# Kernel optimization log

Measured on AMD Instinct MI355X. Metric: run time of the kernel, lower is better.

The kernel has to match this reference:

```python
import jax, jax.numpy as jnp
import numpy as np

N, P, D, C = 2048, 64, 512, 32   # bs*n_vars, patch_num, hidden_dim, cluster_num
H, DFF, L = 8, 2048, 3           # heads, ffn dim, encoder layers
TEMP = 10.0
EPS = 1e-10
LN_EPS = 1e-5


def setup_inputs() -> dict:
    key = jax.random.key(0)
    ks = jax.random.split(key, 18)
    s = 0.02  # small init to keep activations sane
    inp = {}
    inp["input_series"] = jax.random.normal(ks[0], (N, P, D), jnp.float32)
    pi = jax.random.uniform(ks[1], (C,), jnp.float32) + 0.1
    inp["text_pi"] = pi / pi.sum()
    A = jax.random.uniform(ks[2], (C, C), jnp.float32) + 0.1
    inp["text_A"] = A / A.sum(axis=1, keepdims=True)
    # stacked per-layer TransformerEncoderLayer params (torch post-norm, relu)
    inp["qkv_w"] = jax.random.normal(ks[3], (L, 3 * D, D), jnp.float32) * s
    inp["qkv_b"] = jnp.zeros((L, 3 * D), jnp.float32)
    inp["out_w"] = jax.random.normal(ks[4], (L, D, D), jnp.float32) * s
    inp["out_b"] = jnp.zeros((L, D), jnp.float32)
    inp["ln1_w"] = jnp.ones((L, D), jnp.float32)
    inp["ln1_b"] = jnp.zeros((L, D), jnp.float32)
    inp["ff1_w"] = jax.random.normal(ks[5], (L, DFF, D), jnp.float32) * s
    inp["ff1_b"] = jnp.zeros((L, DFF), jnp.float32)
    inp["ff2_w"] = jax.random.normal(ks[6], (L, D, DFF), jnp.float32) * s
    inp["ff2_b"] = jnp.zeros((L, D), jnp.float32)
    inp["ln2_w"] = jnp.ones((L, D), jnp.float32)
    inp["ln2_b"] = jnp.zeros((L, D), jnp.float32)
    inp["mus"] = jax.random.normal(ks[7], (C, D), jnp.float32)
    return inp


def _layer_norm(x, w, b):
    m = x.mean(axis=-1, keepdims=True)
    v = ((x - m) ** 2).mean(axis=-1, keepdims=True)
    return (x - m) * jax.lax.rsqrt(v + LN_EPS) * w + b


def _encoder_layer(x, qkv_w, qkv_b, out_w, out_b, ln1_w, ln1_b,
                   ff1_w, ff1_b, ff2_w, ff2_b, ln2_w, ln2_b):
    n, p, d = x.shape
    dh = d // H
    qkv = x @ qkv_w.T + qkv_b                       # [n,p,3d]
    q, k, v = jnp.split(qkv, 3, axis=-1)
    def split_heads(t):
        return t.reshape(n, p, H, dh).transpose(0, 2, 1, 3)  # [n,h,p,dh]
    q, k, v = split_heads(q), split_heads(k), split_heads(v)
    scores = jnp.einsum('nhqd,nhkd->nhqk', q, k) / (dh ** 0.5)
    attn = jax.nn.softmax(scores, axis=-1)
    o = jnp.einsum('nhqk,nhkd->nhqd', attn, v)
    o = o.transpose(0, 2, 1, 3).reshape(n, p, d)
    o = o @ out_w.T + out_b
    x = _layer_norm(x + o, ln1_w, ln1_b)            # post-norm
    f = jax.nn.relu(x @ ff1_w.T + ff1_b) @ ff2_w.T + ff2_b
    return _layer_norm(x + f, ln2_w, ln2_b)


def reference(input_series, text_pi, text_A, qkv_w, qkv_b, out_w, out_b,
              ln1_w, ln1_b, ff1_w, ff1_b, ff2_w, ff2_b, ln2_w, ln2_b, mus):
    x = input_series
    for l in range(L):
        x = _encoder_layer(x, qkv_w[l], qkv_b[l], out_w[l], out_b[l],
                           ln1_w[l], ln1_b[l], ff1_w[l], ff1_b[l],
                           ff2_w[l], ff2_b[l], ln2_w[l], ln2_b[l])
    emb_ts = x                                       # [N,P,D]
    # ClusterCenters: softmax of exp(-||x - tanh(mu)||^2 / T)
    mu = jnp.tanh(mus)                               # [C,D]
    dist = ((emb_ts ** 2).sum(-1)[..., None]
            + (mu ** 2).sum(-1)[None, None, :]
            - 2.0 * jnp.einsum('npd,cd->npc', emb_ts, mu))  # [N,P,C]
    z = jnp.exp(-dist / TEMP)
    logits_all = z / z.sum(axis=-1, keepdims=True)
    log_za = jnp.log(logits_all + EPS)               # [N,P,C]
    # sequential HMM-style recursion over patches
    l0 = jax.nn.softmax(jnp.log(text_pi + EPS)[None, :] + log_za[:, 0], axis=-1)
    def step(c, lz):
        c2 = jax.nn.softmax(jnp.log(c @ text_A + EPS) + lz, axis=-1)
        return c2, c2
    _, ys = jax.lax.scan(step, l0, jnp.swapaxes(log_za[:, 1:], 0, 1))  # [P-1,N,C]
    cluster_probs = jnp.concatenate([l0[:, None], jnp.swapaxes(ys, 0, 1)], axis=1)
    entropy_loss = -jnp.sum(cluster_probs * jnp.log(cluster_probs + EPS), axis=-1).mean()
    return (cluster_probs, emb_ts, text_pi, text_A, entropy_loss)
```

## Files before the change

kernel.cpp:

```cpp
#include <hip/hip_runtime.h>
#include <stdint.h>


typedef __bf16 bf16;
typedef __bf16 bf16x2 __attribute__((ext_vector_type(2)));
typedef __bf16 bf16x4 __attribute__((ext_vector_type(4)));
typedef __bf16 bf16x8 __attribute__((ext_vector_type(8)));
typedef float  f32x4  __attribute__((ext_vector_type(4)));
typedef float  f32x2  __attribute__((ext_vector_type(2)));

#define EPSF 1e-10f
#define NROWS 131072L

__device__ __forceinline__ float bflo(uint32_t u){ return __uint_as_float(u << 16); }
__device__ __forceinline__ float bfhi(uint32_t u){ return __uint_as_float(u & 0xffff0000u); }

__device__ __forceinline__ void gload_lds16(const bf16* g, bf16* l){
  __builtin_amdgcn_global_load_lds((const __attribute__((address_space(1))) uint32_t*)g,
                                   (__attribute__((address_space(3))) uint32_t*)l,
                                   16, 0, 0);
}

__global__ void k_f2bf(const float* __restrict__ in, bf16* __restrict__ out, long n){
  const long stride = (long)gridDim.x * blockDim.x * 4;
  for (long i = ((long)blockIdx.x * blockDim.x + threadIdx.x) * 4; i < n; i += stride){
    f32x4 v = *(const f32x4*)(in + i);
    bf16x4 o = { (bf16)v[0], (bf16)v[1], (bf16)v[2], (bf16)v[3] };
    *(bf16x4*)(out + i) = o;
  }
}


#define MFMA_HALF(RH)                                                         \
  {                                                                           \
    __builtin_amdgcn_s_setprio(1);                                            \
    _Pragma("unroll")                                                         \
    for (int kk = 0; kk < 2; kk++) {                                          \
      _Pragma("unroll")                                                       \
      for (int i2 = 0; i2 < 4; i2++) {                                        \
        _Pragma("unroll")                                                     \
        for (int jj = 0; jj < 4; jj++) {                                      \
          acc[(RH)*4+i2][jj] = __builtin_amdgcn_mfma_f32_16x16x32_bf16(       \
              a[i2][kk], b[jj][kk], acc[(RH)*4+i2][jj], 0, 0, 0);             \
        }                                                                     \
      }                                                                       \
    }                                                                         \
    __builtin_amdgcn_s_setprio(0);                                            \
  }

#define RD_A(RH)                                                              \
  _Pragma("unroll")                                                           \
  for (int i2 = 0; i2 < 4; i2++) {                                            \
    a[i2][0] = *(const bf16x8*)&Ac[(aRow + (RH)*64 + i2*16) * 64 + sl0];      \
    a[i2][1] = *(const bf16x8*)&Ac[(aRow + (RH)*64 + i2*16) * 64 + sl1];      \
  }

#define RD_B_ALL                                                              \
  _Pragma("unroll")                                                           \
  for (int jj = 0; jj < 4; jj++) {                                            \
    b[jj][0] = *(const bf16x8*)&Bc[(bRow + jj*16) * 64 + sl0];                \
    b[jj][1] = *(const bf16x8*)&Bc[(bRow + jj*16) * 64 + sl1];                \
  }

#define ISSUE_A(dst, BI, KK) \
  gload_lds16(gA + (long)(BI)*64*lda + (KK), (dst) + (BI)*4096 + wslice)
#define ISSUE_B(dst, BI, KK) \
  gload_lds16(gB + (long)(BI)*64*K   + (KK), (dst) + (BI)*4096 + wslice)

#define WAITV(N)  asm volatile("s_waitcnt vmcnt(" #N ")" ::: "memory")
#define WAITL0    asm volatile("s_waitcnt lgkmcnt(0)" ::: "memory")
#define BARRIER   { __builtin_amdgcn_s_barrier(); asm volatile("" ::: "memory"); }

template<int RELU>
__global__ __launch_bounds__(512, 2)
void gemm256(const bf16* __restrict__ A, long lda,
             const bf16* __restrict__ W,
             const float* __restrict__ bias,
             bf16* __restrict__ Cb, long K, int nbx)
{
  const int tid  = threadIdx.x;
  const int wid  = tid >> 6;
  const int lane = tid & 63;
  const int wr = wid >> 2, wc = wid & 3;
  const long ldc = (long)nbx * 256;

  const unsigned nwg = gridDim.x;
  const unsigned q   = nwg >> 3;
  const unsigned swz = (blockIdx.x & 7) * q + (blockIdx.x >> 3);
  const unsigned bx  = swz % (unsigned)nbx;
  const unsigned by  = swz / (unsigned)nbx;
  const long bm = (long)by * 256;
  const long bn = (long)bx * 256;

  __shared__ __align__(16) bf16 smem[65536];
  bf16* const As0 = smem;
  bf16* const Bs0 = smem + 16384;
  bf16* const As1 = smem + 32768;
  bf16* const Bs1 = smem + 49152;

  const int srow   = wid * 8 + (lane >> 3);
  const int scol   = ((lane & 7) ^ ((lane >> 3) & 7)) * 8;
  const int wslice = wid * 512;
  const bf16* gA = A + (bm + srow) * lda + scol;
  const bf16* gB = W + (bn + srow) * K   + scol;

  const int fr = lane & 15, fg = lane >> 4;
  const int aRow = wr * 128 + fr;
  const int bRow = wc * 64  + fr;
  const int sl0 = ((0 + fg) ^ (fr & 7)) * 8;
  const int sl1 = ((4 + fg) ^ (fr & 7)) * 8;

  f32x4 acc[8][4];
#pragma unroll
  for (int i = 0; i < 8; i++)
#pragma unroll
    for (int j = 0; j < 4; j++) acc[i][j] = (f32x4){0.f, 0.f, 0.f, 0.f};

  bf16x8 a[4][2];
  bf16x8 b[4][2];

  const int nt = (int)(K >> 6);

  ISSUE_B(Bs0, 0, 0); ISSUE_B(Bs0, 1, 0); ISSUE_B(Bs0, 2, 0); ISSUE_B(Bs0, 3, 0);
  ISSUE_A(As0, 0, 0); ISSUE_A(As0, 2, 0);
  ISSUE_A(As0, 1, 0); ISSUE_A(As0, 3, 0);
  WAITV(2);
  BARRIER;

  for (int t = 0; t < nt; t++){
    bf16* const Ac = (t & 1) ? As1 : As0;
    bf16* const Bc = (t & 1) ? Bs1 : Bs0;
    bf16* const An = (t & 1) ? As0 : As1;
    bf16* const Bn = (t & 1) ? Bs0 : Bs1;
    const bool stage = (t + 1 < nt);
    const long kn = (long)(t + 1) << 6;

    RD_A(0); RD_B_ALL;
    if (stage){ ISSUE_B(Bn, 0, kn); ISSUE_B(Bn, 1, kn);
                ISSUE_B(Bn, 2, kn); ISSUE_B(Bn, 3, kn);
                ISSUE_A(An, 0, kn); ISSUE_A(An, 2, kn); }
    WAITL0;
    MFMA_HALF(0);
    if (stage){ WAITV(6); } else { WAITV(0); }
    BARRIER;

    RD_A(1);
    if (stage){ ISSUE_A(An, 1, kn); ISSUE_A(An, 3, kn); }
    WAITL0;
    MFMA_HALF(1);
    if (stage){ WAITV(2); }
    BARRIER;
  }

  bf16* const cw = smem + wid * 2304;
  const long strip_row0 = bm + wr * 128;
  const long strip_col0 = bn + wc * 64;
  float bv[4];
#pragma unroll
  for (int j = 0; j < 4; j++) bv[j] = bias[strip_col0 + j * 16 + fr];
  const int rrow = lane >> 3;
  const int rcol = (lane & 7) * 8;

#pragma unroll
  for (int ch = 0; ch < 4; ch++){
#pragma unroll
    for (int i2 = 0; i2 < 2; i2++){
      const int i = ch * 2 + i2;
#pragma unroll
      for (int j = 0; j < 4; j++){
#pragma unroll
        for (int r = 0; r < 4; r++){
          float v = acc[i][j][r] + bv[j];
          if (RELU) v = fmaxf(v, 0.f);
          cw[(i2 * 16 + fg * 4 + r) * 72 + j * 16 + fr] = (bf16)v;
        }
      }
    }
    WAITL0;
#pragma unroll
    for (int p = 0; p < 4; p++){
      const int row = p * 8 + rrow;
      bf16x8 o = *(const bf16x8*)&cw[row * 72 + rcol];
      *(bf16x8*)&Cb[(strip_row0 + ch * 32 + row) * ldc + strip_col0 + rcol] = o;
    }
    WAITL0;
  }
}

__global__ __launch_bounds__(256)
void attention(bf16* __restrict__ qkv)
{
  const int blk = blockIdx.x;
  const long n = blk >> 3;
  const int h  = blk & 7;
  const int tid = threadIdx.x;
  const int wid = tid >> 6, lane = tid & 63;

  __shared__ __align__(16) bf16 Qs[64][72];
  __shared__ __align__(16) bf16 Ks[64][72];
  __shared__ __align__(16) bf16 Vt[64][72];

  bf16* base = qkv + n * 64 * 1536 + h * 64;

  for (int c = tid; c < 512; c += 256){
    const int row = c >> 3, col = (c & 7) * 8;
    const long go = (long)row * 1536 + col;
    *(bf16x8*)&Qs[row][col] = *(const bf16x8*)(base + go);
    *(bf16x8*)&Ks[row][col] = *(const bf16x8*)(base + 512 + go);
    bf16x8 v = *(const bf16x8*)(base + 1024 + go);
#pragma unroll
    for (int e = 0; e < 8; e++) Vt[col + e][row] = v[e];
  }
  __syncthreads();

  const int fr = lane & 15, fg = lane >> 4;
  f32x4 sacc[4];
#pragma unroll
  for (int j = 0; j < 4; j++) sacc[j] = (f32x4){0.f, 0.f, 0.f, 0.f};
#pragma unroll
  for (int ks = 0; ks < 2; ks++){
    bf16x8 aa = *(const bf16x8*)&Qs[wid * 16 + fr][ks * 32 + fg * 8];
#pragma unroll
    for (int j = 0; j < 4; j++){
      bf16x8 bb = *(const bf16x8*)&Ks[j * 16 + fr][ks * 32 + fg * 8];
      sacc[j] = __builtin_amdgcn_mfma_f32_16x16x32_bf16(aa, bb, sacc[j], 0, 0, 0);
    }
  }

  float pv[4][4];
#pragma unroll
  for (int r = 0; r < 4; r++){
    float m = -1e30f;
#pragma unroll
    for (int j = 0; j < 4; j++) m = fmaxf(m, sacc[j][r]);
#pragma unroll
    for (int msk = 1; msk < 16; msk <<= 1) m = fmaxf(m, __shfl_xor(m, msk));
    float s = 0.f;
#pragma unroll
    for (int j = 0; j < 4; j++){
      float p = __expf((sacc[j][r] - m) * 0.125f);
      pv[j][r] = p; s += p;
    }
#pragma unroll
    for (int msk = 1; msk < 16; msk <<= 1) s += __shfl_xor(s, msk);
    const float inv = 1.f / s;
#pragma unroll
    for (int j = 0; j < 4; j++) pv[j][r] *= inv;
  }

#pragma unroll
  for (int j = 0; j < 4; j++)
#pragma unroll
    for (int r = 0; r < 4; r++)
      Qs[wid * 16 + fg * 4 + r][j * 16 + fr] = (bf16)pv[j][r];
  __syncthreads();

  f32x4 oacc[4];
#pragma unroll
  for (int j = 0; j < 4; j++) oacc[j] = (f32x4){0.f, 0.f, 0.f, 0.f};
#pragma unroll
  for (int ks = 0; ks < 2; ks++){
    bf16x8 aa = *(const bf16x8*)&Qs[wid * 16 + fr][ks * 32 + fg * 8];
#pragma unroll
    for (int j = 0; j < 4; j++){
      bf16x8 bb = *(const bf16x8*)&Vt[j * 16 + fr][ks * 32 + fg * 8];
      oacc[j] = __builtin_amdgcn_mfma_f32_16x16x32_bf16(aa, bb, oacc[j], 0, 0, 0);
    }
  }
#pragma unroll
  for (int j = 0; j < 4; j++)
#pragma unroll
    for (int r = 0; r < 4; r++)
      base[(long)(wid * 16 + fg * 4 + r) * 1536 + j * 16 + fr] = (bf16)oacc[j][r];
}

__global__ __launch_bounds__(256)
void resid_ln(const bf16* __restrict__ X, const bf16* __restrict__ O,
              const float* __restrict__ w, const float* __restrict__ b,
              bf16* __restrict__ Y, float* __restrict__ EF)
{
  const int wid = threadIdx.x >> 6, lane = threadIdx.x & 63;
  const long row = (long)blockIdx.x * 4 + wid;
  const uint4 xu = ((const uint4*)(X + row * 512))[lane];
  const uint4 ou = ((const uint4*)(O + row * 512))[lane];
  float s[8];
  s[0] = bflo(xu.x) + bflo(ou.x);  s[1] = bfhi(xu.x) + bfhi(ou.x);
  s[2] = bflo(xu.y) + bflo(ou.y);  s[3] = bfhi(xu.y) + bfhi(ou.y);
  s[4] = bflo(xu.z) + bflo(ou.z);  s[5] = bfhi(xu.z) + bfhi(ou.z);
  s[6] = bflo(xu.w) + bflo(ou.w);  s[7] = bfhi(xu.w) + bfhi(ou.w);
  float sum = 0.f, sq = 0.f;
#pragma unroll
  for (int e = 0; e < 8; e++){ sum += s[e]; sq += s[e] * s[e]; }
#pragma unroll
  for (int m = 1; m < 64; m <<= 1){ sum += __shfl_xor(sum, m); sq += __shfl_xor(sq, m); }
  const float mean = sum * (1.f / 512.f);
  const float var  = sq * (1.f / 512.f) - mean * mean;
  const float rs   = rsqrtf(var + 1e-5f);
  const f32x4 w0 = *(const f32x4*)(w + 8 * lane);
  const f32x4 w1 = *(const f32x4*)(w + 8 * lane + 4);
  const f32x4 b0 = *(const f32x4*)(b + 8 * lane);
  const f32x4 b1 = *(const f32x4*)(b + 8 * lane + 4);
  float o[8];
#pragma unroll
  for (int e = 0; e < 4; e++) o[e]     = (s[e]     - mean) * rs * w0[e] + b0[e];
#pragma unroll
  for (int e = 0; e < 4; e++) o[e + 4] = (s[e + 4] - mean) * rs * w1[e] + b1[e];
  bf16x8 ov = { (bf16)o[0], (bf16)o[1], (bf16)o[2], (bf16)o[3],
                (bf16)o[4], (bf16)o[5], (bf16)o[6], (bf16)o[7] };
  *(bf16x8*)(Y + row * 512 + 8 * lane) = ov;
  if (EF){
    f32x4 e0 = { o[0], o[1], o[2], o[3] };
    f32x4 e1 = { o[4], o[5], o[6], o[7] };
    *(f32x4*)(EF + row * 512 + 8 * lane) = e0;
    *(f32x4*)(EF + row * 512 + 8 * lane + 4) = e1;
  }
}

__global__ __launch_bounds__(256)
void k_mu(const float* __restrict__ mus, bf16* __restrict__ mubf, float* __restrict__ munorm)
{
  const int c = blockIdx.x, tid = threadIdx.x, lane = tid & 63, wid = tid >> 6;
  const f32x2 v = *(const f32x2*)(mus + c * 512 + 2 * tid);
  const float t0 = tanhf(v[0]), t1 = tanhf(v[1]);
  bf16x2 o2 = { (bf16)t0, (bf16)t1 };
  *(bf16x2*)(mubf + c * 512 + 2 * tid) = o2;
  float sq = t0 * t0 + t1 * t1;
#pragma unroll
  for (int m = 1; m < 64; m <<= 1) sq += __shfl_xor(sq, m);
  __shared__ float red[4];
  if (lane == 0) red[wid] = sq;
  __syncthreads();
  if (tid == 0) munorm[c] = red[0] + red[1] + red[2] + red[3];
}

__global__ __launch_bounds__(256)
void cluster_logza(const bf16* __restrict__ X, const bf16* __restrict__ MU,
                   const float* __restrict__ munorm, float* __restrict__ out)
{
  const int tid = threadIdx.x, lane = tid & 63, wid = tid >> 6;
  __shared__ __align__(16) bf16 mus[32][512];
  __shared__ float xs[512];
  __shared__ float red[4];
  __shared__ float dots[32];
  for (int c = tid; c < 2048; c += 256){
    const int r = c >> 6, col = (c & 63) * 8;
    *(bf16x8*)&mus[r][col] = *(const bf16x8*)(MU + r * 512 + col);
  }
  const int cc = tid >> 3, seg = tid & 7;
  const long row0 = (long)blockIdx.x * 16;
  __syncthreads();
  for (int rr = 0; rr < 16; rr++){
    const long row = row0 + rr;
    const uint32_t u = ((const uint32_t*)(X + row * 512))[tid];
    const float aa = bflo(u), bb = bfhi(u);
    xs[2 * tid] = aa; xs[2 * tid + 1] = bb;
    float sq = aa * aa + bb * bb;
#pragma unroll
    for (int m = 1; m < 64; m <<= 1) sq += __shfl_xor(sq, m);
    if (lane == 0) red[wid] = sq;
    __syncthreads();
    const float xn = red[0] + red[1] + red[2] + red[3];
    float p = 0.f;
#pragma unroll
    for (int jj = 0; jj < 8; jj++){
      const int col = jj * 64 + seg * 8;
      bf16x8 m8 = *(const bf16x8*)&mus[cc][col];
      const float* xv = &xs[col];
#pragma unroll
      for (int e = 0; e < 8; e++) p += xv[e] * (float)m8[e];
    }
#pragma unroll
    for (int m = 1; m < 8; m <<= 1) p += __shfl_xor(p, m);
    if (seg == 0) dots[cc] = p;
    __syncthreads();
    if (tid < 32){
      const float dist = xn + munorm[tid] - 2.f * dots[tid];
      const float lg = -dist * 0.1f;
      float mx = lg;
#pragma unroll
      for (int m = 1; m < 32; m <<= 1) mx = fmaxf(mx, __shfl_xor(mx, m, 32));
      const float z = __expf(lg - mx);
      float s = z;
#pragma unroll
      for (int m = 1; m < 32; m <<= 1) s += __shfl_xor(s, m, 32);
      out[row * 32 + tid] = logf(z / s + EPSF);
    }
    __syncthreads();
  }
}

__global__ __launch_bounds__(256)
void k_hmm(const float* __restrict__ lza, const float* __restrict__ pi,
           const float* __restrict__ A, float* __restrict__ cp, float* __restrict__ ent)
{
  __shared__ float As[32][33];
  const int tid = threadIdx.x;
  for (int i = tid; i < 1024; i += 256) As[i >> 5][i & 31] = A[i];
  __syncthreads();
  const int j = tid & 31;
  const long n = (long)blockIdx.x * 8 + (tid >> 5);
  const float* lz = lza + n * 2048;

  float c = logf(pi[j] + EPSF) + lz[j];
  {
    float mx = c;
#pragma unroll
    for (int m = 1; m < 32; m <<= 1) mx = fmaxf(mx, __shfl_xor(mx, m, 32));
    float z = __expf(c - mx), s = z;
#pragma unroll
    for (int m = 1; m < 32; m <<= 1) s += __shfl_xor(s, m, 32);
    c = z / s;
  }
  cp[n * 2048 + j] = c;
  float ea = -c * logf(c + EPSF);

  for (int p = 1; p < 64; p++){
    float y = 0.f;
#pragma unroll
    for (int i = 0; i < 32; i++) y += __shfl(c, i, 32) * As[i][j];
    float t = logf(y + EPSF) + lz[p * 32 + j];
    float mx = t;
#pragma unroll
    for (int m = 1; m < 32; m <<= 1) mx = fmaxf(mx, __shfl_xor(mx, m, 32));
    float z = __expf(t - mx), s = z;
#pragma unroll
    for (int m = 1; m < 32; m <<= 1) s += __shfl_xor(s, m, 32);
    c = z / s;
    cp[n * 2048 + p * 32 + j] = c;
    ea += -c * logf(c + EPSF);
  }
#pragma unroll
  for (int m = 1; m < 32; m <<= 1) ea += __shfl_xor(ea, m, 32);
  if (j == 0) atomicAdd(ent, ea * (1.f / 131072.f));
}

extern "C" void kernel_launch(void* const* d_in, const int* in_sizes, int n_in,
                              void* d_out, int out_size, void* d_ws, size_t ws_size,
                              hipStream_t stream)
{
  (void)in_sizes; (void)n_in; (void)out_size; (void)ws_size;
  const float* in_series = (const float*)d_in[0];
  const float* pi    = (const float*)d_in[1];
  const float* Amat  = (const float*)d_in[2];
  const float* qkv_w = (const float*)d_in[3];
  const float* qkv_b = (const float*)d_in[4];
  const float* out_w = (const float*)d_in[5];
  const float* out_b = (const float*)d_in[6];
  const float* ln1_w = (const float*)d_in[7];
  const float* ln1_b = (const float*)d_in[8];
  const float* ff1_w = (const float*)d_in[9];
  const float* ff1_b = (const float*)d_in[10];
  const float* ff2_w = (const float*)d_in[11];
  const float* ff2_b = (const float*)d_in[12];
  const float* ln2_w = (const float*)d_in[13];
  const float* ln2_b = (const float*)d_in[14];
  const float* mus   = (const float*)d_in[15];

  char* ws = (char*)d_ws;
  bf16* region0 = (bf16*)(ws);
  bf16* xb      = (bf16*)(ws + 536870912L);
  bf16* oproj   = (bf16*)(ws + 671088640L);
  bf16* w_qkv   = (bf16*)(ws + 805306368L);
  bf16* w_out   = (bf16*)(ws + 810024960L);
  bf16* w_ff1   = (bf16*)(ws + 811597824L);
  bf16* w_ff2   = (bf16*)(ws + 817889280L);
  bf16* mubf    = (bf16*)(ws + 824180736L);
  float* munorm = (float*)(ws + 824213504L);
  float* logza  = (float*)(ws);

  float* out_f = (float*)d_out;
  float* cp    = out_f;
  float* emb   = out_f + 4194304L;
  float* o_pi  = out_f + 71303168L;
  float* o_A   = out_f + 71303200L;
  float* o_ent = out_f + 71304224L;

  k_f2bf<<<8192, 256, 0, stream>>>(in_series, xb, 67108864L);
  k_f2bf<<<1024, 256, 0, stream>>>(qkv_w, w_qkv, 2359296L);
  k_f2bf<<<1024, 256, 0, stream>>>(out_w, w_out, 786432L);
  k_f2bf<<<1024, 256, 0, stream>>>(ff1_w, w_ff1, 3145728L);
  k_f2bf<<<1024, 256, 0, stream>>>(ff2_w, w_ff2, 3145728L);
  k_mu<<<32, 256, 0, stream>>>(mus, mubf, munorm);

  for (int l = 0; l < 3; l++){
    gemm256<0><<<3072, 512, 0, stream>>>(xb, 512, w_qkv + (long)l * 786432L,
                                         qkv_b + (long)l * 1536, region0, 512, 6);
    attention<<<16384, 256, 0, stream>>>(region0);
    gemm256<0><<<1024, 512, 0, stream>>>(region0, 1536, w_out + (long)l * 262144L,
                                         out_b + (long)l * 512, oproj, 512, 2);
    resid_ln<<<32768, 256, 0, stream>>>(xb, oproj, ln1_w + (long)l * 512,
                                        ln1_b + (long)l * 512, xb, nullptr);
    gemm256<1><<<4096, 512, 0, stream>>>(xb, 512, w_ff1 + (long)l * 1048576L,
                                         ff1_b + (long)l * 2048, region0, 512, 8);
    gemm256<0><<<1024, 512, 0, stream>>>(region0, 2048, w_ff2 + (long)l * 1048576L,
                                         ff2_b + (long)l * 512, oproj, 2048, 2);
    resid_ln<<<32768, 256, 0, stream>>>(xb, oproj, ln2_w + (long)l * 512,
                                        ln2_b + (long)l * 512, xb,
                                        (l == 2) ? emb : nullptr);
  }

  cluster_logza<<<8192, 256, 0, stream>>>(xb, mubf, munorm, logza);
  hipMemsetAsync(o_ent, 0, 4, stream);
  k_hmm<<<256, 256, 0, stream>>>(logza, pi, Amat, cp, o_ent);
  hipMemcpyAsync(o_pi, pi, 32 * sizeof(float), hipMemcpyDeviceToDevice, stream);
  hipMemcpyAsync(o_A, Amat, 1024 * sizeof(float), hipMemcpyDeviceToDevice, stream);
}
```

Measured before the change: 3.963 ms.

## Use 4 waves with 128x128 warp tiles in the 256x256 GEMM

The 256x256 GEMM block goes from 8 waves (each 128x64) to 4 waves (each 128x128), so each wave holds a 8x8 grid of MFMA accumulators and reuses every A fragment across twice as many B fragments. The global-to-LDS staging is reorganised so each wave issues its own set of row chunks, with new vmcnt wait counts, and the epilogue staging buffer is widened. The aim is fewer LDS reads per MFMA. In exchange it raises register pressure (256 accumulator floats per lane) and drops occupancy to one 256-thread block per CU, which risks less latency hiding.

```diff
diff --git a/kernel.cpp b/kernel.cpp
--- a/kernel.cpp
+++ b/kernel.cpp
@@ -31,7 +31,7 @@
 }
 
 
-#define MFMA_HALF(RH)                                                         \
+#define MFMA_BLK(IB)                                                          \
   {                                                                           \
     __builtin_amdgcn_s_setprio(1);                                            \
     _Pragma("unroll")                                                         \
@@ -39,9 +39,9 @@
       _Pragma("unroll")                                                       \
       for (int i2 = 0; i2 < 4; i2++) {                                        \
         _Pragma("unroll")                                                     \
-        for (int jj = 0; jj < 4; jj++) {                                      \
-          acc[(RH)*4+i2][jj] = __builtin_amdgcn_mfma_f32_16x16x32_bf16(       \
-              a[i2][kk], b[jj][kk], acc[(RH)*4+i2][jj], 0, 0, 0);             \
+        for (int j2 = 0; j2 < 8; j2++) {                                      \
+          acc[(IB)*4+i2][j2] = __builtin_amdgcn_mfma_f32_16x16x32_bf16(       \
+              a[i2][kk], b[j2][kk], acc[(IB)*4+i2][j2], 0, 0, 0);             \
         }                                                                     \
       }                                                                       \
     }                                                                         \
@@ -51,28 +51,28 @@
 #define RD_A(RH)                                                              \
   _Pragma("unroll")                                                           \
   for (int i2 = 0; i2 < 4; i2++) {                                            \
-    a[i2][0] = *(const bf16x8*)&Ac[(aRow + (RH)*64 + i2*16) * 64 + sl0];      \
-    a[i2][1] = *(const bf16x8*)&Ac[(aRow + (RH)*64 + i2*16) * 64 + sl1];      \
+    a[i2][0] = *(const bf16x8*)&Ac[aOff + ((RH)*4 + i2)*1024 + sl0];          \
+    a[i2][1] = *(const bf16x8*)&Ac[aOff + ((RH)*4 + i2)*1024 + sl1];          \
   }
 
 #define RD_B_ALL                                                              \
   _Pragma("unroll")                                                           \
-  for (int jj = 0; jj < 4; jj++) {                                            \
-    b[jj][0] = *(const bf16x8*)&Bc[(bRow + jj*16) * 64 + sl0];                \
-    b[jj][1] = *(const bf16x8*)&Bc[(bRow + jj*16) * 64 + sl1];                \
-  }
-
-#define ISSUE_A(dst, BI, KK) \
-  gload_lds16(gA + (long)(BI)*64*lda + (KK), (dst) + (BI)*4096 + wslice)
-#define ISSUE_B(dst, BI, KK) \
-  gload_lds16(gB + (long)(BI)*64*K   + (KK), (dst) + (BI)*4096 + wslice)
+  for (int j2 = 0; j2 < 8; j2++) {                                            \
+    b[j2][0] = *(const bf16x8*)&Bc[bOff + j2*1024 + sl0];                     \
+    b[j2][1] = *(const bf16x8*)&Bc[bOff + j2*1024 + sl1];                     \
+  }
+
+#define ISSUE_A(dst, C, KK) \
+  gload_lds16(gA + (long)(C)*8*lda + (KK), (dst) + (C)*512)
+#define ISSUE_B(dst, C, KK) \
+  gload_lds16(gB + (long)(C)*8*K   + (KK), (dst) + (C)*512)
 
 #define WAITV(N)  asm volatile("s_waitcnt vmcnt(" #N ")" ::: "memory")
 #define WAITL0    asm volatile("s_waitcnt lgkmcnt(0)" ::: "memory")
 #define BARRIER   { __builtin_amdgcn_s_barrier(); asm volatile("" ::: "memory"); }
 
 template<int RELU>
-__global__ __launch_bounds__(512, 2)
+__global__ __launch_bounds__(256, 1)
 void gemm256(const bf16* __restrict__ A, long lda,
              const bf16* __restrict__ W,
              const float* __restrict__ bias,
@@ -81,7 +81,7 @@
   const int tid  = threadIdx.x;
   const int wid  = tid >> 6;
   const int lane = tid & 63;
-  const int wr = wid >> 2, wc = wid & 3;
+  const int wr = wid >> 1, wc = wid & 1;
   const long ldc = (long)nbx * 256;
 
   const unsigned nwg = gridDim.x;
@@ -98,33 +98,37 @@
   bf16* const As1 = smem + 32768;
   bf16* const Bs1 = smem + 49152;
 
-  const int srow   = wid * 8 + (lane >> 3);
-  const int scol   = ((lane & 7) ^ ((lane >> 3) & 7)) * 8;
-  const int wslice = wid * 512;
-  const bf16* gA = A + (bm + srow) * lda + scol;
-  const bf16* gB = W + (bn + srow) * K   + scol;
+  const int gsrc = ((lane & 7) ^ ((lane >> 3) & 7)) * 8;
+  const bf16* gA = A + (bm + (lane >> 3)) * lda + gsrc;
+  const bf16* gB = W + (bn + (lane >> 3)) * K   + gsrc;
+
+  const int cA0[4] = { 2*wid, 2*wid + 1, 16 + 2*wid, 17 + 2*wid };
+  const int cA1[4] = { 8 + 2*wid, 9 + 2*wid, 24 + 2*wid, 25 + 2*wid };
 
   const int fr = lane & 15, fg = lane >> 4;
-  const int aRow = wr * 128 + fr;
-  const int bRow = wc * 64  + fr;
+  const int aOff = (wr * 128 + fr) * 64;
+  const int bOff = (wc * 128 + fr) * 64;
   const int sl0 = ((0 + fg) ^ (fr & 7)) * 8;
   const int sl1 = ((4 + fg) ^ (fr & 7)) * 8;
 
-  f32x4 acc[8][4];
+  f32x4 acc[8][8];
 #pragma unroll
   for (int i = 0; i < 8; i++)
 #pragma unroll
-    for (int j = 0; j < 4; j++) acc[i][j] = (f32x4){0.f, 0.f, 0.f, 0.f};
+    for (int j = 0; j < 8; j++) acc[i][j] = (f32x4){0.f, 0.f, 0.f, 0.f};
 
   bf16x8 a[4][2];
-  bf16x8 b[4][2];
+  bf16x8 b[8][2];
 
   const int nt = (int)(K >> 6);
 
-  ISSUE_B(Bs0, 0, 0); ISSUE_B(Bs0, 1, 0); ISSUE_B(Bs0, 2, 0); ISSUE_B(Bs0, 3, 0);
-  ISSUE_A(As0, 0, 0); ISSUE_A(As0, 2, 0);
-  ISSUE_A(As0, 1, 0); ISSUE_A(As0, 3, 0);
-  WAITV(2);
+#pragma unroll
+  for (int u = 0; u < 4; u++) ISSUE_A(As0, cA0[u], 0);
+#pragma unroll
+  for (int u = 0; u < 8; u++) ISSUE_B(Bs0, 8*wid + u, 0);
+#pragma unroll
+  for (int u = 0; u < 4; u++) ISSUE_A(As0, cA1[u], 0);
+  WAITV(4);
   BARRIER;
 
   for (int t = 0; t < nt; t++){
@@ -136,30 +140,32 @@
     const long kn = (long)(t + 1) << 6;
 
     RD_A(0); RD_B_ALL;
-    if (stage){ ISSUE_B(Bn, 0, kn); ISSUE_B(Bn, 1, kn);
-                ISSUE_B(Bn, 2, kn); ISSUE_B(Bn, 3, kn);
-                ISSUE_A(An, 0, kn); ISSUE_A(An, 2, kn); }
-    WAITL0;
-    MFMA_HALF(0);
-    if (stage){ WAITV(6); } else { WAITV(0); }
+    if (stage){
+#pragma unroll
+      for (int u = 0; u < 4; u++) ISSUE_A(An, cA0[u], kn);
+#pragma unroll
+      for (int u = 0; u < 8; u++) ISSUE_B(Bn, 8*wid + u, kn);
+    }
+    MFMA_BLK(0);
+    if (stage){ WAITV(12); } else { WAITV(0); }
     BARRIER;
 
     RD_A(1);
-    if (stage){ ISSUE_A(An, 1, kn); ISSUE_A(An, 3, kn); }
-    WAITL0;
-    MFMA_HALF(1);
-    if (stage){ WAITV(2); }
+    if (stage){
+#pragma unroll
+      for (int u = 0; u < 4; u++) ISSUE_A(An, cA1[u], kn);
+    }
+    MFMA_BLK(1);
+    if (stage){ WAITV(4); } else { WAITV(0); }
     BARRIER;
   }
 
-  bf16* const cw = smem + wid * 2304;
-  const long strip_row0 = bm + wr * 128;
-  const long strip_col0 = bn + wc * 64;
-  float bv[4];
-#pragma unroll
-  for (int j = 0; j < 4; j++) bv[j] = bias[strip_col0 + j * 16 + fr];
-  const int rrow = lane >> 3;
-  const int rcol = (lane & 7) * 8;
+  bf16* const cw = smem + wid * 4352;
+  const long r0 = bm + wr * 128;
+  const long c0 = bn + wc * 128;
+  float bv[8];
+#pragma unroll
+  for (int j = 0; j < 8; j++) bv[j] = bias[c0 + j * 16 + fr];
 
 #pragma unroll
   for (int ch = 0; ch < 4; ch++){
@@ -167,21 +173,21 @@
     for (int i2 = 0; i2 < 2; i2++){
       const int i = ch * 2 + i2;
 #pragma unroll
-      for (int j = 0; j < 4; j++){
+      for (int j = 0; j < 8; j++){
 #pragma unroll
         for (int r = 0; r < 4; r++){
           float v = acc[i][j][r] + bv[j];
           if (RELU) v = fmaxf(v, 0.f);
-          cw[(i2 * 16 + fg * 4 + r) * 72 + j * 16 + fr] = (bf16)v;
+          cw[(i2 * 16 + fg * 4 + r) * 136 + j * 16 + fr] = (bf16)v;
         }
       }
     }
     WAITL0;
 #pragma unroll
-    for (int p = 0; p < 4; p++){
-      const int row = p * 8 + rrow;
-      bf16x8 o = *(const bf16x8*)&cw[row * 72 + rcol];
-      *(bf16x8*)&Cb[(strip_row0 + ch * 32 + row) * ldc + strip_col0 + rcol] = o;
+    for (int p = 0; p < 8; p++){
+      const int row = p * 4 + fg;
+      bf16x8 o = *(const bf16x8*)&cw[row * 136 + fr * 8];
+      *(bf16x8*)&Cb[(r0 + ch * 32 + row) * ldc + c0 + fr * 8] = o;
     }
     WAITL0;
   }
@@ -483,16 +489,16 @@
   k_mu<<<32, 256, 0, stream>>>(mus, mubf, munorm);
 
   for (int l = 0; l < 3; l++){
-    gemm256<0><<<3072, 512, 0, stream>>>(xb, 512, w_qkv + (long)l * 786432L,
+    gemm256<0><<<3072, 256, 0, stream>>>(xb, 512, w_qkv + (long)l * 786432L,
                                          qkv_b + (long)l * 1536, region0, 512, 6);
     attention<<<16384, 256, 0, stream>>>(region0);
-    gemm256<0><<<1024, 512, 0, stream>>>(region0, 1536, w_out + (long)l * 262144L,
+    gemm256<0><<<1024, 256, 0, stream>>>(region0, 1536, w_out + (long)l * 262144L,
                                          out_b + (long)l * 512, oproj, 512, 2);
     resid_ln<<<32768, 256, 0, stream>>>(xb, oproj, ln1_w + (long)l * 512,
                                         ln1_b + (long)l * 512, xb, nullptr);
-    gemm256<1><<<4096, 512, 0, stream>>>(xb, 512, w_ff1 + (long)l * 1048576L,
+    gemm256<1><<<4096, 256, 0, stream>>>(xb, 512, w_ff1 + (long)l * 1048576L,
                                          ff1_b + (long)l * 2048, region0, 512, 8);
-    gemm256<0><<<1024, 512, 0, stream>>>(region0, 2048, w_ff2 + (long)l * 1048576L,
+    gemm256<0><<<1024, 256, 0, stream>>>(region0, 2048, w_ff2 + (long)l * 1048576L,
                                          ff2_b + (long)l * 512, oproj, 2048, 2);
     resid_ln<<<32768, 256, 0, stream>>>(xb, oproj, ln2_w + (long)l * 512,
                                         ln2_b + (long)l * 512, xb,
```

Result: slower. 4.192 ms (+5.8%).
